# Kernel optimization log

Hardware: AMD Instinct MI355X
Metric: run time of the kernel (lower is better)

Reference implementation:

```python
import jax, jax.numpy as jnp
import numpy as np


def _gcn_conv(x, src, dst, W, b, n_nodes):
    # PyG GCNConv: add self-loops, symmetric normalization D^-1/2 A D^-1/2,
    # linear transform, scatter-add aggregation, bias.
    loop = jnp.arange(n_nodes, dtype=src.dtype)
    s = jnp.concatenate([src, loop])
    d = jnp.concatenate([dst, loop])
    deg = jax.ops.segment_sum(jnp.ones_like(s, dtype=x.dtype), d, num_segments=n_nodes)
    dinv = jnp.where(deg > 0, jax.lax.rsqrt(deg), 0.0)
    norm = dinv[s] * dinv[d]                      # [E+N]
    h = x @ W                                     # [N, H] dense GEMM
    msg = h[s] * norm[:, None]                    # [E+N, H] gathered messages
    out = jax.ops.segment_sum(msg, d, num_segments=n_nodes)  # scatter-add
    return out + b


def setup_inputs() -> dict:
    key = jax.random.key(0)
    ks = jax.random.split(key, 8)
    n_nodes, n_edges, d_in, hidden, num_graphs = 10000, 160000, 512, 512, 64
    x = jax.random.normal(ks[0], (n_nodes, d_in), dtype=jnp.float32)
    edge_index = jax.random.randint(ks[1], (2, n_edges), 0, n_nodes, dtype=jnp.int64)
    batch = jnp.sort(jax.random.randint(ks[2], (n_nodes,), 0, num_graphs, dtype=jnp.int64))
    # Xavier-uniform-ish weights (GCNConv lin has no bias separate in newer PyG; keep W+b per layer)
    def xavier(k, shape):
        fan_in, fan_out = shape[0], shape[1]
        lim = np.sqrt(6.0 / (fan_in + fan_out))
        return jax.random.uniform(k, shape, jnp.float32, -lim, lim)
    W1 = xavier(ks[3], (d_in, hidden))
    b1 = jnp.zeros((hidden,), jnp.float32)
    W2 = xavier(ks[4], (hidden, hidden))
    b2 = jnp.zeros((hidden,), jnp.float32)
    Wlin = xavier(ks[5], (hidden, 1))
    blin = jnp.zeros((1,), jnp.float32)
    return {"x": x, "edge_index": edge_index, "batch": batch, "num_graphs": num_graphs,
            "W1": W1, "b1": b1, "W2": W2, "b2": b2, "Wlin": Wlin, "blin": blin}


def reference(x, edge_index, batch, num_graphs, W1, b1, W2, b2, Wlin, blin):
    n_nodes = x.shape[0]
    src, dst = edge_index[0], edge_index[1]
    h = _gcn_conv(x, src, dst, W1, b1, n_nodes)
    h = jax.nn.relu(h)
    h = _gcn_conv(h, src, dst, W2, b2, n_nodes)
    pooled = jax.ops.segment_sum(h, batch, num_segments=num_graphs)  # global_add_pool
    return pooled @ Wlin + blin  # [num_graphs, 1]
```

## Files before the change

### kernel.cpp

```cpp
#include <hip/hip_runtime.h>
#include <stdint.h>

typedef __attribute__((ext_vector_type(8))) short s16x8;
typedef __attribute__((ext_vector_type(8))) unsigned short u16x8;
typedef __attribute__((ext_vector_type(4))) float f32x4;

#define D 512
#define BM 128
#define BK 64
#define CAP 96

__device__ __forceinline__ unsigned short f2bf(float f) {
    unsigned u = __float_as_uint(f);
    return (unsigned short)((u + 0x7FFFu + ((u >> 16) & 1u)) >> 16);
}
__device__ __forceinline__ float bf2f(unsigned short h) {
    return __uint_as_float(((unsigned)h) << 16);
}

__global__ __launch_bounds__(256) void k_prep(const float* W1, int* fill, float* z,
                                              unsigned short* w1t, int nN) {
    int b = blockIdx.x, t = threadIdx.x;
    if (b < 64) {
        __shared__ float tile[64][65];
        int ti = b >> 3, tj = b & 7;
#pragma unroll
        for (int p = 0; p < 4; ++p) {
            int r = p * 16 + (t >> 4);
            int c = (t & 15) * 4;
            float4 v = *(const float4*)(W1 + (size_t)(ti * 64 + r) * D + tj * 64 + c);
            tile[r][c] = v.x; tile[r][c + 1] = v.y; tile[r][c + 2] = v.z; tile[r][c + 3] = v.w;
        }
        __syncthreads();
        int c = t >> 2;
        int r0 = (t & 3) * 16;
        u16x8 o0, o1;
#pragma unroll
        for (int i = 0; i < 8; ++i) o0[i] = f2bf(tile[r0 + i][c]);
#pragma unroll
        for (int i = 0; i < 8; ++i) o1[i] = f2bf(tile[r0 + 8 + i][c]);
        unsigned short* wp = w1t + (size_t)(tj * 64 + c) * D + ti * 64 + r0;
        *(u16x8*)wp = o0;
        *(u16x8*)(wp + 8) = o1;
    } else {
        int i = (b - 64) * 256 + t;
        if (i < nN) { fill[i] = 0; z[i] = 0.f; }
    }
}

__global__ __launch_bounds__(256) void k_gemm_scatter(const float* X, const unsigned short* BT,
                                                      unsigned short* C, int Mreal,
                                                      const int* src, const int* dst,
                                                      int* fill, int* csr_src, int nE,
                                                      const float* W2, const float* Wlin,
                                                      const float* b2, const float* blin,
                                                      float* w2l, float* out, int nG) {
    __shared__ __align__(16) unsigned short smem[4 * BM * BK];
    int b = blockIdx.x;
    int t = threadIdx.x;
    if (b >= 316) {
        int br = b - 316;
        if (br < 625) {
            int e = br * 256 + t;
            if (e < nE) {
                int s = src[e], d = dst[e];
                int pos = atomicAdd(&fill[d], 1);
                if (pos < CAP) csr_src[(size_t)d * CAP + pos] = s;
            }
        } else if (br < 754) {
            int i = (br - 625) * 4 + (t >> 6);
            int l = t & 63;
            if (i < D + 1) {
                const float* row = (i < D) ? (W2 + (size_t)i * D) : b2;
                float4 a0 = *(const float4*)(row + l * 8);
                float4 a1 = *(const float4*)(row + l * 8 + 4);
                float4 c0 = *(const float4*)(Wlin + l * 8);
                float4 c1 = *(const float4*)(Wlin + l * 8 + 4);
                float p = a0.x * c0.x + a0.y * c0.y + a0.z * c0.z + a0.w * c0.w
                        + a1.x * c1.x + a1.y * c1.y + a1.z * c1.z + a1.w * c1.w;
#pragma unroll
                for (int o = 32; o > 0; o >>= 1) p += __shfl_xor(p, o);
                if (l == 0) w2l[i] = p;
            }
        } else {
            if (t < nG) out[t] = blin[0];
        }
        return;
    }
    int tn0 = (b & 3) * BM, tm0 = (b >> 2) * BM;
    int lane = t & 63, wave = t >> 6;
    int wr = wave >> 1, wc = wave & 1;
    f32x4 acc[4][4] = {};
    int r15 = lane & 15;
    int khalf = lane >> 4;

    int a_row[4], a_kg[4];
    const float* a_gp_base[4];
#pragma unroll
    for (int i = 0; i < 4; ++i) {
        int idx = t + 256 * i;
        a_row[i] = idx >> 3; a_kg[i] = idx & 7;
        int grow = tm0 + a_row[i]; if (grow >= Mreal) grow = Mreal - 1;
        a_gp_base[i] = X + (size_t)grow * D + a_kg[i] * 8;
    }

    auto issue_B = [&](unsigned short* Bsbuf, int k0) {
        int rb0 = wave * 8;
#pragma unroll
        for (int c = 0; c < 4; ++c) {
            int rbase = c * 32 + rb0;
            int row = rbase + (lane >> 3);
            int kg = (lane & 7) ^ (row & 7);
            const unsigned short* gsrc = BT + (size_t)(tn0 + row) * D + k0 + kg * 8;
            __builtin_amdgcn_global_load_lds(
                (const __attribute__((address_space(1))) unsigned int*)gsrc,
                (__attribute__((address_space(3))) unsigned int*)(Bsbuf + rbase * BK),
                16, 0, 0);
        }
    };

    float4 af0[4], af1[4];
    auto load_A = [&](int k0) {
#pragma unroll
        for (int i = 0; i < 4; ++i) {
            const float* gp = a_gp_base[i] + k0;
            af0[i] = *(const float4*)gp;
            af1[i] = *(const float4*)(gp + 4);
        }
    };
    auto write_A = [&](unsigned short* Asbuf) {
#pragma unroll
        for (int i = 0; i < 4; ++i) {
            u16x8 o;
            o[0] = f2bf(af0[i].x); o[1] = f2bf(af0[i].y); o[2] = f2bf(af0[i].z); o[3] = f2bf(af0[i].w);
            o[4] = f2bf(af1[i].x); o[5] = f2bf(af1[i].y); o[6] = f2bf(af1[i].z); o[7] = f2bf(af1[i].w);
            *(u16x8*)&Asbuf[a_row[i] * BK + (a_kg[i] ^ (a_row[i] & 7)) * 8] = o;
        }
    };

    issue_B(smem + 2 * BM * BK, 0);
    load_A(0);
    write_A(smem);
    __syncthreads();

    int cur = 0;
    for (int k0 = 0; k0 < D; k0 += BK) {
        unsigned short* Asc = smem + cur * BM * BK;
        unsigned short* Bsc = smem + (2 + cur) * BM * BK;
        if (k0 + BK < D) {
            issue_B(smem + (2 + (cur ^ 1)) * BM * BK, k0 + BK);
            load_A(k0 + BK);
        }
#pragma unroll
        for (int ks = 0; ks < 2; ++ks) {
            int g = ks * 4 + khalf;
            s16x8 a[4], bb[4];
#pragma unroll
            for (int m = 0; m < 4; ++m) {
                int row = wr * 64 + m * 16 + r15;
                a[m] = *(const s16x8*)&Asc[row * BK + (g ^ (row & 7)) * 8];
            }
#pragma unroll
            for (int n = 0; n < 4; ++n) {
                int row = wc * 64 + n * 16 + r15;
                bb[n] = *(const s16x8*)&Bsc[row * BK + (g ^ (row & 7)) * 8];
            }
#pragma unroll
            for (int m = 0; m < 4; ++m)
#pragma unroll
                for (int n = 0; n < 4; ++n)
                    acc[m][n] = __builtin_amdgcn_mfma_f32_16x16x32_bf16(a[m], bb[n], acc[m][n], 0, 0, 0);
        }
        if (k0 + BK < D) write_A(smem + (cur ^ 1) * BM * BK);
        __syncthreads();
        cur ^= 1;
    }

    int cr = (lane >> 4) * 4;
    int cc = lane & 15;
#pragma unroll
    for (int m = 0; m < 4; ++m)
#pragma unroll
        for (int n = 0; n < 4; ++n)
#pragma unroll
            for (int r = 0; r < 4; ++r)
                smem[(wr * 64 + m * 16 + cr + r) * 132 + wc * 64 + n * 16 + cc] = f2bf(acc[m][n][r]);
    __syncthreads();
#pragma unroll
    for (int it = 0; it < 8; ++it) {
        int row = it * 16 + (t >> 4);
        int c8 = (t & 15) * 8;
        int grow = tm0 + row;
        if (grow < Mreal) {
            u16x8 vv = *(const u16x8*)&smem[row * 132 + c8];
            *(u16x8*)&C[(size_t)grow * D + tn0 + c8] = vv;
        }
    }
}

__global__ __launch_bounds__(256) void k_agg1(const unsigned short* h1b, const int* csr_src,
                                              const int* fill, const float* b1,
                                              const float* w2l, float* z, int nN) {
    int bid = blockIdx.x;
    int xcd = bid & 7;
    int slice = xcd >> 1;
    int chunk = (bid >> 3) * 2 + (xcd & 1);
    int t = threadIdx.x;
    int g = t >> 4;
    int l = t & 15;
    int v = chunk * 16 + g;
    if (v >= nN) return;
    int f0 = (slice << 7) + l * 8;

    float acc[8];
    float4 ba = *(const float4*)(b1 + f0);
    float4 bb = *(const float4*)(b1 + f0 + 4);
    acc[0] = ba.x; acc[1] = ba.y; acc[2] = ba.z; acc[3] = ba.w;
    acc[4] = bb.x; acc[5] = bb.y; acc[6] = bb.z; acc[7] = bb.w;

    int deg = fill[v];
    float degv1 = (float)(deg + 1);
    float wself = 1.0f / degv1;
    u16x8 hv = *(const u16x8*)(h1b + (size_t)v * D + f0);
#pragma unroll
    for (int j = 0; j < 8; ++j) acc[j] += wself * bf2f(hv[j]);

    const int* row = csr_src + (size_t)v * CAP;
    int sb = (g & 3) << 4;
    for (int eb = 0; eb < deg; eb += 16) {
        int n = deg - eb; if (n > 16) n = 16;
        int myi = 0; float myw = 0.f;
        if (l < n) {
            myi = row[eb + l];
            myw = rsqrtf((float)(fill[myi] + 1) * degv1);
        }
        int j = 0;
        for (; j + 4 <= n; j += 4) {
            int s0 = __shfl(myi, sb + j),     s1 = __shfl(myi, sb + j + 1);
            int s2 = __shfl(myi, sb + j + 2), s3 = __shfl(myi, sb + j + 3);
            float w0 = __shfl(myw, sb + j),     w1 = __shfl(myw, sb + j + 1);
            float w2 = __shfl(myw, sb + j + 2), w3 = __shfl(myw, sb + j + 3);
            u16x8 h0 = *(const u16x8*)(h1b + (size_t)s0 * D + f0);
            u16x8 h1 = *(const u16x8*)(h1b + (size_t)s1 * D + f0);
            u16x8 h2 = *(const u16x8*)(h1b + (size_t)s2 * D + f0);
            u16x8 h3 = *(const u16x8*)(h1b + (size_t)s3 * D + f0);
#pragma unroll
            for (int q = 0; q < 8; ++q) acc[q] += w0 * bf2f(h0[q]);
#pragma unroll
            for (int q = 0; q < 8; ++q) acc[q] += w1 * bf2f(h1[q]);
#pragma unroll
            for (int q = 0; q < 8; ++q) acc[q] += w2 * bf2f(h2[q]);
#pragma unroll
            for (int q = 0; q < 8; ++q) acc[q] += w3 * bf2f(h3[q]);
        }
        for (; j < n; ++j) {
            int s = __shfl(myi, sb + j);
            float w = __shfl(myw, sb + j);
            u16x8 hs = *(const u16x8*)(h1b + (size_t)s * D + f0);
#pragma unroll
            for (int q = 0; q < 8; ++q) acc[q] += w * bf2f(hs[q]);
        }
    }

    float4 wa = *(const float4*)(w2l + f0);
    float4 wb = *(const float4*)(w2l + f0 + 4);
    float wv[8] = {wa.x, wa.y, wa.z, wa.w, wb.x, wb.y, wb.z, wb.w};
    float p = 0.f;
#pragma unroll
    for (int j = 0; j < 8; ++j) p += fmaxf(acc[j], 0.f) * wv[j];
    p += __shfl_xor(p, 8);
    p += __shfl_xor(p, 4);
    p += __shfl_xor(p, 2);
    p += __shfl_xor(p, 1);
    if (l == 0) atomicAdd(&z[v], p);
}

__global__ __launch_bounds__(256) void k_agg2(const float* z, const int* src, const int* dst,
                                              const int* fill, const float* w2l,
                                              const int* batch, float* out, int nN, int nE, int nG) {
    __shared__ float bins[64];
    int t = threadIdx.x;
    if (t < 64) bins[t] = 0.f;
    __syncthreads();
    int i = blockIdx.x * 256 + t;
    if (i < nE) {
        int s = src[i], d = dst[i];
        float val = rsqrtf((float)(fill[s] + 1) * (float)(fill[d] + 1)) * z[s];
        int g = batch[d];
        if (g < 64) atomicAdd(&bins[g], val); else atomicAdd(&out[g], val);
    }
    if (i < nN) {
        float val = w2l[D] + z[i] / (float)(fill[i] + 1);
        int g = batch[i];
        if (g < 64) atomicAdd(&bins[g], val); else atomicAdd(&out[g], val);
    }
    __syncthreads();
    if (t < 64 && t < nG) {
        float v = bins[t];
        if (v != 0.f) atomicAdd(&out[t], v);
    }
}

extern "C" void kernel_launch(void* const* d_in, const int* in_sizes, int n_in,
                              void* d_out, int out_size, void* d_ws, size_t ws_size,
                              hipStream_t stream) {
    const float* x    = (const float*)d_in[0];
    const int*   ei   = (const int*)d_in[1];
    const int*   batch= (const int*)d_in[2];
    const float* W1   = (const float*)d_in[4];
    const float* b1   = (const float*)d_in[5];
    const float* W2   = (const float*)d_in[6];
    const float* b2   = (const float*)d_in[7];
    const float* Wlin = (const float*)d_in[8];
    const float* blin = (const float*)d_in[9];
    float* out = (float*)d_out;

    int nN = in_sizes[0] / D;
    int nE = in_sizes[1] / 2;
    int nG = out_size;
    const int* src = ei;
    const int* dst = ei + nE;

    char* p = (char*)d_ws;
    auto alloc = [&](size_t b) { char* r = p; p += (b + 255) & ~(size_t)255; return (void*)r; };
    int*   fill    = (int*)alloc((size_t)nN * 4);
    int*   csr_src = (int*)alloc((size_t)nN * CAP * 4);
    float* z       = (float*)alloc((size_t)nN * 4);
    float* w2l     = (float*)alloc((size_t)(D + 1) * 4);
    unsigned short* w1t = (unsigned short*)alloc((size_t)D * D * 2);
    unsigned short* h1b = (unsigned short*)alloc((size_t)nN * D * 2);

    k_prep<<<104, 256, 0, stream>>>(W1, fill, z, w1t, nN);
    int nb = 316 + (nE + 255) / 256 + 129 + 1;
    k_gemm_scatter<<<nb, 256, 0, stream>>>(x, w1t, h1b, nN, src, dst, fill, csr_src, nE,
                                           W2, Wlin, b2, blin, w2l, out, nG);
    k_agg1<<<313 * 8, 256, 0, stream>>>(h1b, csr_src, fill, b1, w2l, z, nN);
    nb = (nE + 255) / 256;
    k_agg2<<<nb, 256, 0, stream>>>(z, src, dst, fill, w2l, batch, out, nN, nE, nG);
}
```

Baseline: 67.97 us.

## Fuse W1 transpose and bf16 conversion into GEMM B-tile loading

Removes the separate k_prep kernel that transposed W1 into a bf16 buffer. The GEMM now reads fp32 W1 directly with strided per-thread loads, converts to bf16 in registers and writes swizzled tiles to LDS. The fill and z counters are zeroed with one hipMemsetAsync over a contiguous region. This saves a kernel launch and an intermediate buffer. In exchange, the B loads are now scalar and strided, and every GEMM block redoes the W1 conversion instead of using async global-to-LDS loads.

```diff
diff --git a/kernel.cpp b/kernel.cpp
--- a/kernel.cpp
+++ b/kernel.cpp
@@ -18,37 +18,8 @@
     return __uint_as_float(((unsigned)h) << 16);
 }
 
-__global__ __launch_bounds__(256) void k_prep(const float* W1, int* fill, float* z,
-                                              unsigned short* w1t, int nN) {
-    int b = blockIdx.x, t = threadIdx.x;
-    if (b < 64) {
-        __shared__ float tile[64][65];
-        int ti = b >> 3, tj = b & 7;
-#pragma unroll
-        for (int p = 0; p < 4; ++p) {
-            int r = p * 16 + (t >> 4);
-            int c = (t & 15) * 4;
-            float4 v = *(const float4*)(W1 + (size_t)(ti * 64 + r) * D + tj * 64 + c);
-            tile[r][c] = v.x; tile[r][c + 1] = v.y; tile[r][c + 2] = v.z; tile[r][c + 3] = v.w;
-        }
-        __syncthreads();
-        int c = t >> 2;
-        int r0 = (t & 3) * 16;
-        u16x8 o0, o1;
-#pragma unroll
-        for (int i = 0; i < 8; ++i) o0[i] = f2bf(tile[r0 + i][c]);
-#pragma unroll
-        for (int i = 0; i < 8; ++i) o1[i] = f2bf(tile[r0 + 8 + i][c]);
-        unsigned short* wp = w1t + (size_t)(tj * 64 + c) * D + ti * 64 + r0;
-        *(u16x8*)wp = o0;
-        *(u16x8*)(wp + 8) = o1;
-    } else {
-        int i = (b - 64) * 256 + t;
-        if (i < nN) { fill[i] = 0; z[i] = 0.f; }
-    }
-}
-
-__global__ __launch_bounds__(256) void k_gemm_scatter(const float* X, const unsigned short* BT,
+__global__ __launch_bounds__(256) void k_gemm_scatter(const float* __restrict__ X,
+                                                      const float* __restrict__ W1,
                                                       unsigned short* C, int Mreal,
                                                       const int* src, const int* dst,
                                                       int* fill, int* csr_src, int nE,
@@ -103,29 +74,29 @@
         int grow = tm0 + a_row[i]; if (grow >= Mreal) grow = Mreal - 1;
         a_gp_base[i] = X + (size_t)grow * D + a_kg[i] * 8;
     }
-
-    auto issue_B = [&](unsigned short* Bsbuf, int k0) {
-        int rb0 = wave * 8;
-#pragma unroll
-        for (int c = 0; c < 4; ++c) {
-            int rbase = c * 32 + rb0;
-            int row = rbase + (lane >> 3);
-            int kg = (lane & 7) ^ (row & 7);
-            const unsigned short* gsrc = BT + (size_t)(tn0 + row) * D + k0 + kg * 8;
-            __builtin_amdgcn_global_load_lds(
-                (const __attribute__((address_space(1))) unsigned int*)gsrc,
-                (__attribute__((address_space(3))) unsigned int*)(Bsbuf + rbase * BK),
-                16, 0, 0);
-        }
-    };
+    int b_n[4], b_kg[4];
+#pragma unroll
+    for (int p = 0; p < 4; ++p) {
+        int idx = t + 256 * p;
+        b_n[p] = idx & 127; b_kg[p] = idx >> 7;
+    }
 
     float4 af0[4], af1[4];
+    float bf[4][8];
     auto load_A = [&](int k0) {
 #pragma unroll
         for (int i = 0; i < 4; ++i) {
             const float* gp = a_gp_base[i] + k0;
             af0[i] = *(const float4*)gp;
             af1[i] = *(const float4*)(gp + 4);
+        }
+    };
+    auto load_B = [&](int k0) {
+#pragma unroll
+        for (int p = 0; p < 4; ++p) {
+            const float* gp = W1 + (size_t)(k0 + b_kg[p] * 8) * D + tn0 + b_n[p];
+#pragma unroll
+            for (int j = 0; j < 8; ++j) bf[p][j] = gp[(size_t)j * D];
         }
     };
     auto write_A = [&](unsigned short* Asbuf) {
@@ -137,9 +108,19 @@
             *(u16x8*)&Asbuf[a_row[i] * BK + (a_kg[i] ^ (a_row[i] & 7)) * 8] = o;
         }
     };
-
-    issue_B(smem + 2 * BM * BK, 0);
+    auto write_B = [&](unsigned short* Bsbuf) {
+#pragma unroll
+        for (int p = 0; p < 4; ++p) {
+            u16x8 o;
+#pragma unroll
+            for (int j = 0; j < 8; ++j) o[j] = f2bf(bf[p][j]);
+            *(u16x8*)&Bsbuf[b_n[p] * BK + ((b_kg[p] ^ (b_n[p] & 7)) << 3)] = o;
+        }
+    };
+
+    load_B(0);
     load_A(0);
+    write_B(smem + 2 * BM * BK);
     write_A(smem);
     __syncthreads();
 
@@ -148,7 +129,7 @@
         unsigned short* Asc = smem + cur * BM * BK;
         unsigned short* Bsc = smem + (2 + cur) * BM * BK;
         if (k0 + BK < D) {
-            issue_B(smem + (2 + (cur ^ 1)) * BM * BK, k0 + BK);
+            load_B(k0 + BK);
             load_A(k0 + BK);
         }
 #pragma unroll
@@ -171,7 +152,10 @@
                 for (int n = 0; n < 4; ++n)
                     acc[m][n] = __builtin_amdgcn_mfma_f32_16x16x32_bf16(a[m], bb[n], acc[m][n], 0, 0, 0);
         }
-        if (k0 + BK < D) write_A(smem + (cur ^ 1) * BM * BK);
+        if (k0 + BK < D) {
+            write_B(smem + (2 + (cur ^ 1)) * BM * BK);
+            write_A(smem + (cur ^ 1) * BM * BK);
+        }
         __syncthreads();
         cur ^= 1;
     }
@@ -323,16 +307,17 @@
 
     char* p = (char*)d_ws;
     auto alloc = [&](size_t b) { char* r = p; p += (b + 255) & ~(size_t)255; return (void*)r; };
-    int*   fill    = (int*)alloc((size_t)nN * 4);
+    int*   fz      = (int*)alloc((size_t)nN * 8);
+    int*   fill    = fz;
+    float* z       = (float*)(fz + nN);
     int*   csr_src = (int*)alloc((size_t)nN * CAP * 4);
-    float* z       = (float*)alloc((size_t)nN * 4);
     float* w2l     = (float*)alloc((size_t)(D + 1) * 4);
-    unsigned short* w1t = (unsigned short*)alloc((size_t)D * D * 2);
     unsigned short* h1b = (unsigned short*)alloc((size_t)nN * D * 2);
 
-    k_prep<<<104, 256, 0, stream>>>(W1, fill, z, w1t, nN);
+    hipMemsetAsync(fz, 0, (size_t)nN * 8, stream);
+
     int nb = 316 + (nE + 255) / 256 + 129 + 1;
-    k_gemm_scatter<<<nb, 256, 0, stream>>>(x, w1t, h1b, nN, src, dst, fill, csr_src, nE,
+    k_gemm_scatter<<<nb, 256, 0, stream>>>(x, W1, h1b, nN, src, dst, fill, csr_src, nE,
                                            W2, Wlin, b2, blin, w2l, out, nG);
     k_agg1<<<313 * 8, 256, 0, stream>>>(h1b, csr_src, fill, b1, w2l, z, nN);
     nb = (nE + 255) / 256;
```

New measurement: 69.54 us. 2.3% more time.
